# Kernel optimization log

Measured on AMD Instinct MI355X. Metric: run time of the kernel, lower is better.

The kernel has to match this reference:

```python
import jax, jax.numpy as jnp
import numpy as np


def setup_inputs() -> dict:
    key = jax.random.key(0)
    k1, k2 = jax.random.split(key)
    B, G = 32, 512
    center = jax.random.normal(k1, (B, G, 6), dtype=jnp.float32)
    lrf = jax.random.normal(k2, (B, G, 3, 3), dtype=jnp.float32)
    return {"center": center, "lrf": lrf}


def reference(center, lrf):
    # center: [B, G, 6], lrf: [B, G, 3, 3]
    center_pos = center[:, :, 0:3]                       # [B, G, 3]
    # diff[b, i, j, c] = center_pos[b, j, c] - center_pos[b, i, c]
    diff = center_pos[:, None, :, :] - center_pos[:, :, None, :]  # [B, G, G, 3]
    # rel_pos[b, i, j, k] = sum_c diff[b, i, j, c] * lrf[b, i, c, k]
    rel_pos = jnp.einsum('bijc,bick->bijk', diff, lrf)   # [B, G, G, 3]
    # rel_ori[b, i, j] = lrf[b, i]^T @ lrf[b, j]
    rel_ori = jnp.einsum('bikm,bjkn->bijmn', lrf, lrf)   # [B, G, G, 3, 3]
    return (rel_pos, rel_ori)
```

## Files before the change

kernel.cpp:

```cpp
#include <hip/hip_runtime.h>


#define G_ 512
#define NB 32

__global__ __launch_bounds__(256, 8) void relposori_kernel(
    const float* __restrict__ center,
    const float* __restrict__ lrf,
    float* __restrict__ out_pos,
    float* __restrict__ out_ori)
{
    __shared__ float s[4 * 768];
    int tid  = threadIdx.x;
    int lane = tid & 63;
    int w    = tid >> 6;
    float* sp = s + w * 768;
    float* so = sp + 192;

    const int nchunks = NB * G_ * 8;
    const int nwaves  = 2048 * 4;
    int wave_id = __builtin_amdgcn_readfirstlane(blockIdx.x * 4 + w);

    for (int c = wave_id; c < nchunks; c += nwaves) {
        int bi = c >> 3;
        int b  = bi >> 9;
        int q  = c & 7;
        int j0 = q << 6;

        const float* ci = center + (size_t)bi * 6;
        const float* li = lrf    + (size_t)bi * 9;
        float ci0 = ci[0], ci1 = ci[1], ci2 = ci[2];
        float li_[9];
#pragma unroll
        for (int t = 0; t < 9; ++t) li_[t] = li[t];

        int j = j0 + lane;
        size_t bj = (size_t)b * G_ + (size_t)j;
        const float* cj = center + bj * 6;
        const float* lj = lrf    + bj * 9;
        float d0 = cj[0] - ci0, d1 = cj[1] - ci1, d2 = cj[2] - ci2;
        float lj_[9];
#pragma unroll
        for (int t = 0; t < 9; ++t) lj_[t] = lj[t];

#pragma unroll
        for (int k = 0; k < 3; ++k)
            sp[lane * 3 + k] = d0 * li_[k] + d1 * li_[3 + k] + d2 * li_[6 + k];

#pragma unroll
        for (int m = 0; m < 3; ++m)
#pragma unroll
            for (int n = 0; n < 3; ++n)
                so[lane * 9 + m * 3 + n] = li_[m]     * lj_[n]
                                         + li_[3 + m] * lj_[3 + n]
                                         + li_[6 + m] * lj_[6 + n];

        asm volatile("s_waitcnt lgkmcnt(0)" ::: "memory");
        __builtin_amdgcn_sched_barrier(0);

        const float4* sp4 = (const float4*)sp;
        const float4* so4 = (const float4*)so;
        float4* op4 = (float4*)out_pos + ((size_t)bi * 384 + 48 * q);
        float4* oo4 = (float4*)out_ori + ((size_t)bi * 1152 + 144 * q);

        if (lane < 48) op4[lane] = sp4[lane];
        oo4[lane]      = so4[lane];
        oo4[64 + lane] = so4[64 + lane];
        if (lane < 16) oo4[128 + lane] = so4[128 + lane];

        asm volatile("" ::: "memory");
        __builtin_amdgcn_wave_barrier();
    }
}

extern "C" void kernel_launch(void* const* d_in, const int* in_sizes, int n_in,
                              void* d_out, int out_size, void* d_ws, size_t ws_size,
                              hipStream_t stream) {
    const float* center = (const float*)d_in[0];
    const float* lrf    = (const float*)d_in[1];
    float* out = (float*)d_out;

    const int B = 32;
    const size_t n_pos = (size_t)B * G_ * G_ * 3;
    float* out_pos = out;
    float* out_ori = out + n_pos;

    dim3 grid(2048);
    dim3 block(256);
    hipLaunchKernelGGL(relposori_kernel, grid, block, 0, stream,
                       center, lrf, out_pos, out_ori);
}
```

Measured before the change: 80.68 us.

## Compute outputs per row with lane-mapped direct global stores, dropping LDS staging

```diff
diff --git a/kernel.cpp b/kernel.cpp
--- a/kernel.cpp
+++ b/kernel.cpp
@@ -10,66 +10,73 @@
     float* __restrict__ out_pos,
     float* __restrict__ out_ori)
 {
-    __shared__ float s[4 * 768];
     int tid  = threadIdx.x;
     int lane = tid & 63;
     int w    = tid >> 6;
-    float* sp = s + w * 768;
-    float* so = sp + 192;
-
-    const int nchunks = NB * G_ * 8;
-    const int nwaves  = 2048 * 4;
     int wave_id = __builtin_amdgcn_readfirstlane(blockIdx.x * 4 + w);
 
-    for (int c = wave_id; c < nchunks; c += nwaves) {
-        int bi = c >> 3;
-        int b  = bi >> 9;
-        int q  = c & 7;
-        int j0 = q << 6;
+    int jj9 = lane / 9, c9 = lane % 9;
+    int m   = c9 / 3,   n  = c9 % 3;
+    int jj3 = lane / 3, c3 = lane % 3;
 
-        const float* ci = center + (size_t)bi * 6;
-        const float* li = lrf    + (size_t)bi * 9;
-        float ci0 = ci[0], ci1 = ci[1], ci2 = ci[2];
+    for (int rr = 0; rr < 2; ++rr) {
+        int r = wave_id * 2 + rr;
+        int b = r >> 9;
+
+        const float* li = lrf + (size_t)r * 9;
         float li_[9];
 #pragma unroll
         for (int t = 0; t < 9; ++t) li_[t] = li[t];
+        const float* ci = center + (size_t)r * 6;
+        float ci0 = ci[0], ci1 = ci[1], ci2 = ci[2];
 
-        int j = j0 + lane;
-        size_t bj = (size_t)b * G_ + (size_t)j;
-        const float* cj = center + bj * 6;
-        const float* lj = lrf    + bj * 9;
-        float d0 = cj[0] - ci0, d1 = cj[1] - ci1, d2 = cj[2] - ci2;
-        float lj_[9];
-#pragma unroll
-        for (int t = 0; t < 9; ++t) lj_[t] = lj[t];
+        float A0 = (m == 0) ? li_[0] : (m == 1) ? li_[1] : li_[2];
+        float A1 = (m == 0) ? li_[3] : (m == 1) ? li_[4] : li_[5];
+        float A2 = (m == 0) ? li_[6] : (m == 1) ? li_[7] : li_[8];
+        float P0 = (c3 == 0) ? li_[0] : (c3 == 1) ? li_[1] : li_[2];
+        float P1 = (c3 == 0) ? li_[3] : (c3 == 1) ? li_[4] : li_[5];
+        float P2 = (c3 == 0) ? li_[6] : (c3 == 1) ? li_[7] : li_[8];
 
-#pragma unroll
-        for (int k = 0; k < 3; ++k)
-            sp[lane * 3 + k] = d0 * li_[k] + d1 * li_[3 + k] + d2 * li_[6 + k];
+        const float* lb = lrf    + (size_t)b * (G_ * 9);
+        const float* cb = center + (size_t)b * (G_ * 6);
+        float* orow = out_ori + (size_t)r * (G_ * 9);
+        float* prow = out_pos + (size_t)r * (G_ * 3);
 
-#pragma unroll
-        for (int m = 0; m < 3; ++m)
-#pragma unroll
-            for (int n = 0; n < 3; ++n)
-                so[lane * 9 + m * 3 + n] = li_[m]     * lj_[n]
-                                         + li_[3 + m] * lj_[3 + n]
-                                         + li_[6 + m] * lj_[6 + n];
+        if (lane < 63) {
+            int offc = jj3 * 6;
+#pragma unroll 4
+            for (int j0 = 0; j0 < 504; j0 += 21) {
+                const float* p = cb + j0 * 6;
+                float d0 = p[offc]     - ci0;
+                float d1 = p[offc + 1] - ci1;
+                float d2 = p[offc + 2] - ci2;
+                prow[j0 * 3 + lane] = d0 * P0 + d1 * P1 + d2 * P2;
+            }
+            if (lane < 24) {
+                const float* p = cb + 504 * 6;
+                float d0 = p[offc]     - ci0;
+                float d1 = p[offc + 1] - ci1;
+                float d2 = p[offc + 2] - ci2;
+                prow[504 * 3 + lane] = d0 * P0 + d1 * P1 + d2 * P2;
+            }
 
-        asm volatile("s_waitcnt lgkmcnt(0)" ::: "memory");
-        __builtin_amdgcn_sched_barrier(0);
-
-        const float4* sp4 = (const float4*)sp;
-        const float4* so4 = (const float4*)so;
-        float4* op4 = (float4*)out_pos + ((size_t)bi * 384 + 48 * q);
-        float4* oo4 = (float4*)out_ori + ((size_t)bi * 1152 + 144 * q);
-
-        if (lane < 48) op4[lane] = sp4[lane];
-        oo4[lane]      = so4[lane];
-        oo4[64 + lane] = so4[64 + lane];
-        if (lane < 16) oo4[128 + lane] = so4[128 + lane];
-
-        asm volatile("" ::: "memory");
-        __builtin_amdgcn_wave_barrier();
+            int offo = jj9 * 9 + n;
+#pragma unroll 4
+            for (int j0 = 0; j0 < 511; j0 += 7) {
+                const float* p = lb + j0 * 9;
+                float b0 = p[offo];
+                float b1 = p[offo + 3];
+                float b2 = p[offo + 6];
+                orow[j0 * 9 + lane] = A0 * b0 + A1 * b1 + A2 * b2;
+            }
+            if (lane < 9) {
+                const float* p = lb + 511 * 9;
+                float b0 = p[n];
+                float b1 = p[n + 3];
+                float b2 = p[n + 6];
+                orow[511 * 9 + lane] = A0 * b0 + A1 * b1 + A2 * b2;
+            }
+        }
     }
 }
 
```

After: 143.8 us. 1.78x slower.
